# Kernel tuning notes

Measured on AMD Instinct MI355X. Metric: run time of the kernel, lower is better.

Reference implementation:

```python
import jax, jax.numpy as jnp
import numpy as np

SCALE = 0.125  # 1/sqrt(d_k), d_k = 64


def setup_inputs() -> dict:
    key = jax.random.key(0)
    kq, kk, kv, kp = jax.random.split(key, 4)
    H, B, L, T, D = 16, 4, 1024, 1024, 64
    return {
        "query": jax.random.normal(kq, (H, B, L, D), dtype=jnp.float32),
        "key": jax.random.normal(kk, (H, B, T, D), dtype=jnp.float32),
        "value": jax.random.normal(kv, (H, B, T, D), dtype=jnp.float32),
        "prev_attention": jax.random.normal(kp, (H, B, L, T), dtype=jnp.float32),
    }


def reference(query, key, value, prev_attention):
    # scores: [h, b, l, t]
    scores = jnp.einsum("hblk,hbtk->hblt", query, key) * SCALE
    scores = scores + prev_attention
    attention = jax.nn.softmax(scores, axis=-1)
    # dropout disabled (rate 0.0) for deterministic reference
    output = jnp.einsum("hblt,hbtv->hblv", attention, value)
    return (output, attention)
```

## Files before the change

kernel.cpp:

```cpp
#include <hip/hip_runtime.h>

#define SCALE 0.125f

constexpr int L_ = 1024, T_ = 1024, D_ = 64, HB_ = 64;

using f32x4 = __attribute__((ext_vector_type(4))) float;
using half8 = __attribute__((ext_vector_type(8))) _Float16;
using half4 = __attribute__((ext_vector_type(4))) _Float16;

__global__ __launch_bounds__(256) void cvt_k(const float* __restrict__ k,
                                             _Float16* __restrict__ kh) {
  const size_t i = ((size_t)blockIdx.x * 256 + threadIdx.x) * 8;
  f32x4 a = *(const f32x4*)(k + i);
  f32x4 b = *(const f32x4*)(k + i + 4);
  half8 h;
#pragma unroll
  for (int e = 0; e < 4; ++e) {
    h[e] = (_Float16)a[e];
    h[4 + e] = (_Float16)b[e];
  }
  *(half8*)(kh + i) = h;
}

__global__ __launch_bounds__(256) void cvt_v(const float* __restrict__ v,
                                             _Float16* __restrict__ vh) {
  __shared__ _Float16 ts[64][136];
  const int tid = threadIdx.x;
  const int hb = blockIdx.y;
  const int t0 = blockIdx.x * 128;
  {
    const int tr = tid >> 1, dh = (tid & 1) * 32;
    const float* p = v + ((size_t)hb * T_ + t0 + tr) * D_ + dh;
#pragma unroll
    for (int i = 0; i < 8; ++i) {
      f32x4 r = *(const f32x4*)(p + i * 4);
#pragma unroll
      for (int e = 0; e < 4; ++e) ts[dh + i * 4 + e][tr] = (_Float16)r[e];
    }
  }
  __syncthreads();
  {
    const int d = tid >> 2, tq = (tid & 3) * 32;
    _Float16* qo = vh + ((size_t)hb * D_ + d) * T_ + t0 + tq;
#pragma unroll
    for (int i = 0; i < 4; ++i)
      *(half8*)(qo + i * 8) = *(const half8*)&ts[d][tq + i * 8];
  }
}

__global__ __launch_bounds__(512) void zpass(
    const float* __restrict__ q, const _Float16* __restrict__ Kh,
    const float* __restrict__ prev, float* __restrict__ out,
    float* __restrict__ att) {
  __shared__ __align__(16) _Float16 Ks[1024][70];
  __shared__ __align__(16) _Float16 El[8][16][72];

  const int ltile = blockIdx.x;
  const int hb    = blockIdx.y;
  const int tid = threadIdx.x;
  const int w = tid >> 6, l = tid & 63, l15 = l & 15, lg = l >> 4;
  const int qrow = ltile * 128 + w * 16 + l15;

  const _Float16* kbase = Kh + (size_t)hb * T_ * D_;

  {
    const int srow = tid >> 2, scol = (tid & 3) * 16;
#pragma unroll
    for (int rep = 0; rep < 8; ++rep) {
      const int r = rep * 128 + srow;
      half8 a = *(const half8*)(kbase + (size_t)r * D_ + scol);
      half8 b = *(const half8*)(kbase + (size_t)r * D_ + scol + 8);
      *(half8*)&Ks[r][scol] = a;
      *(half8*)&Ks[r][scol + 8] = b;
    }
  }

  half8 qb2[2];
  {
    const float* qp = q + ((size_t)hb * L_ + qrow) * D_ + lg * 8;
#pragma unroll
    for (int f = 0; f < 2; ++f)
#pragma unroll
      for (int e = 0; e < 8; ++e) qb2[f][e] = (_Float16)qp[f * 32 + e];
  }

  const float* prow = prev + ((size_t)hb * L_ + qrow) * (size_t)T_;
  const int cr = l >> 2, j = l & 3;
  _Float16* eprow =
      (_Float16*)(att +
                  ((size_t)hb * L_ + ltile * 128 + w * 16 + cr) * (size_t)T_) +
      T_;

  f32x4 pb[2][4];
  auto pload = [&](int c, int s) {
#pragma unroll
    for (int nt = 0; nt < 4; ++nt)
      pb[s][nt] = *(const f32x4*)(prow + c * 64 + nt * 16 + lg * 4);
  };
  pload(0, 0);
  pload(1, 1);

  __syncthreads();

  float zsum = 0.f;

#pragma unroll 2
  for (int c = 0; c < 16; ++c) {
    f32x4 pvv[4];
#pragma unroll
    for (int nt = 0; nt < 4; ++nt) pvv[nt] = pb[c & 1][nt];
    if (c < 14) pload(c + 2, c & 1);

#pragma unroll
    for (int nt = 0; nt < 4; ++nt) {
      const int trow = c * 64 + nt * 16 + l15;
      half8 ka0 = *(const half8*)&Ks[trow][lg * 8];
      half8 ka1 = *(const half8*)&Ks[trow][32 + lg * 8];
      f32x4 acc = {0.f, 0.f, 0.f, 0.f};
      acc = __builtin_amdgcn_mfma_f32_16x16x32_f16(ka0, qb2[0], acc, 0, 0, 0);
      acc = __builtin_amdgcn_mfma_f32_16x16x32_f16(ka1, qb2[1], acc, 0, 0, 0);

      float e0 = __expf(acc[0] * SCALE + pvv[nt][0]);
      float e1 = __expf(acc[1] * SCALE + pvv[nt][1]);
      float e2 = __expf(acc[2] * SCALE + pvv[nt][2]);
      float e3 = __expf(acc[3] * SCALE + pvv[nt][3]);
      zsum += (e0 + e1) + (e2 + e3);
      half4 ev;
      ev[0] = (_Float16)e0; ev[1] = (_Float16)e1;
      ev[2] = (_Float16)e2; ev[3] = (_Float16)e3;
      *(half4*)&El[w][l15][nt * 16 + lg * 4] = ev;
    }

    half8 ha = *(const half8*)&El[w][cr][j * 8];
    half8 hb2 = *(const half8*)&El[w][cr][32 + j * 8];
    *(half8*)(eprow + c * 64 + j * 8) = ha;
    *(half8*)(eprow + c * 64 + 32 + j * 8) = hb2;
  }

  zsum += __shfl_xor(zsum, 16, 64);
  zsum += __shfl_xor(zsum, 32, 64);
  if (lg == 0) out[((size_t)hb * L_ + qrow) * (size_t)D_] = 1.0f / zsum;
}

__global__ __launch_bounds__(512) void pvpass(
    const _Float16* __restrict__ Vh, float* __restrict__ out,
    float* __restrict__ att) {
  __shared__ __align__(16) _Float16 Vt[64][1030];

  const int ltile = blockIdx.x;
  const int hb    = blockIdx.y;
  const int tid = threadIdx.x;
  const int w = tid >> 6, l = tid & 63, l15 = l & 15, lg = l >> 4;
  const int qrow = ltile * 128 + w * 16 + l15;

  const _Float16* vbh = Vh + (size_t)hb * D_ * T_;

  {
    const int d = tid >> 3, tq = (tid & 7) * 8;
#pragma unroll
    for (int rep = 0; rep < 16; ++rep) {
      const int t = rep * 64 + tq;
      *(half8*)&Vt[d][t] = *(const half8*)(vbh + (size_t)d * T_ + t);
    }
  }

  float* arow = att + ((size_t)hb * L_ + qrow) * (size_t)T_;
  const _Float16* erow = (const _Float16*)arow + T_;
  const float rzq = out[((size_t)hb * L_ + qrow) * (size_t)D_];

  half8 eb[4][2];
  auto eload = [&](int c, int s) {
    eb[s][0] = *(const half8*)(erow + c * 64 + lg * 8);
    eb[s][1] = *(const half8*)(erow + c * 64 + 32 + lg * 8);
  };
  eload(0, 0); eload(1, 1); eload(2, 2); eload(3, 3);

  __syncthreads();

  f32x4 oacc[4];
#pragma unroll
  for (int nd = 0; nd < 4; ++nd) oacc[nd] = (f32x4){0.f, 0.f, 0.f, 0.f};

#pragma unroll 4
  for (int c = 0; c < 16; ++c) {
    half8 e0 = eb[c & 3][0], e1 = eb[c & 3][1];
    if (c < 12) eload(c + 4, c & 3);

#pragma unroll
    for (int ks = 0; ks < 2; ++ks) {
      half8 ef = ks ? e1 : e0;
      f32x4 s0, s1;
      half8 af;
#pragma unroll
      for (int e = 0; e < 4; ++e) {
        float v0 = (float)ef[e] * rzq;
        float v1 = (float)ef[4 + e] * rzq;
        s0[e] = v0; s1[e] = v1;
        af[e] = (_Float16)v0;
        af[4 + e] = (_Float16)v1;
      }
      *(f32x4*)(arow + c * 64 + ks * 32 + lg * 8) = s0;
      *(f32x4*)(arow + c * 64 + ks * 32 + lg * 8 + 4) = s1;

#pragma unroll
      for (int nd = 0; nd < 4; ++nd) {
        half8 vb =
            *(const half8*)&Vt[nd * 16 + l15][c * 64 + ks * 32 + lg * 8];
        oacc[nd] =
            __builtin_amdgcn_mfma_f32_16x16x32_f16(af, vb, oacc[nd], 0, 0, 0);
      }
    }
  }

  float* outw =
      out + ((size_t)hb * L_ + ltile * 128 + w * 16 + lg * 4) * (size_t)D_;
#pragma unroll
  for (int nd = 0; nd < 4; ++nd)
#pragma unroll
    for (int i = 0; i < 4; ++i)
      outw[(size_t)i * D_ + nd * 16 + l15] = oacc[nd][i];
}

extern "C" void kernel_launch(void* const* d_in, const int* in_sizes, int n_in,
                              void* d_out, int out_size, void* d_ws,
                              size_t ws_size, hipStream_t stream) {
  const float* q    = (const float*)d_in[0];
  const float* k    = (const float*)d_in[1];
  const float* v    = (const float*)d_in[2];
  const float* prev = (const float*)d_in[3];

  float* out = (float*)d_out;
  float* att = out + (size_t)HB_ * L_ * D_;

  const size_t KV_ELEMS = (size_t)HB_ * T_ * D_;
  _Float16* Kh = (_Float16*)d_ws;
  _Float16* Vh = Kh + KV_ELEMS;

  cvt_k<<<(int)(KV_ELEMS / (256 * 8)), 256, 0, stream>>>(k, Kh);
  cvt_v<<<dim3(T_ / 128, HB_), 256, 0, stream>>>(v, Vh);

  zpass<<<dim3(L_ / 128, HB_), 512, 0, stream>>>(q, Kh, prev, out, att);
  pvpass<<<dim3(L_ / 128, HB_), 512, 0, stream>>>(Vh, out, att);
}
```

Before: 259.1 us.

## Fuse softmax-normalize and PV into one two-pass kernel, fold K conversion in

New measurement: 228.0 us. 1.14x faster.

```diff
diff --git a/kernel.cpp b/kernel.cpp
--- a/kernel.cpp
+++ b/kernel.cpp
@@ -7,20 +7,6 @@
 using f32x4 = __attribute__((ext_vector_type(4))) float;
 using half8 = __attribute__((ext_vector_type(8))) _Float16;
 using half4 = __attribute__((ext_vector_type(4))) _Float16;
-
-__global__ __launch_bounds__(256) void cvt_k(const float* __restrict__ k,
-                                             _Float16* __restrict__ kh) {
-  const size_t i = ((size_t)blockIdx.x * 256 + threadIdx.x) * 8;
-  f32x4 a = *(const f32x4*)(k + i);
-  f32x4 b = *(const f32x4*)(k + i + 4);
-  half8 h;
-#pragma unroll
-  for (int e = 0; e < 4; ++e) {
-    h[e] = (_Float16)a[e];
-    h[4 + e] = (_Float16)b[e];
-  }
-  *(half8*)(kh + i) = h;
-}
 
 __global__ __launch_bounds__(256) void cvt_v(const float* __restrict__ v,
                                              _Float16* __restrict__ vh) {
@@ -48,10 +34,10 @@
   }
 }
 
-__global__ __launch_bounds__(512) void zpass(
-    const float* __restrict__ q, const _Float16* __restrict__ Kh,
-    const float* __restrict__ prev, float* __restrict__ out,
-    float* __restrict__ att) {
+__global__ __launch_bounds__(512) void attn_all(
+    const float* __restrict__ q, const float* __restrict__ kk,
+    const _Float16* __restrict__ Vh, const float* __restrict__ prev,
+    float* __restrict__ out, float* __restrict__ att) {
   __shared__ __align__(16) _Float16 Ks[1024][70];
   __shared__ __align__(16) _Float16 El[8][16][72];
 
@@ -61,17 +47,25 @@
   const int w = tid >> 6, l = tid & 63, l15 = l & 15, lg = l >> 4;
   const int qrow = ltile * 128 + w * 16 + l15;
 
-  const _Float16* kbase = Kh + (size_t)hb * T_ * D_;
-
   {
     const int srow = tid >> 2, scol = (tid & 3) * 16;
+    const float* kp0 = kk + (size_t)hb * T_ * D_;
 #pragma unroll
     for (int rep = 0; rep < 8; ++rep) {
       const int r = rep * 128 + srow;
-      half8 a = *(const half8*)(kbase + (size_t)r * D_ + scol);
-      half8 b = *(const half8*)(kbase + (size_t)r * D_ + scol + 8);
-      *(half8*)&Ks[r][scol] = a;
-      *(half8*)&Ks[r][scol + 8] = b;
+      const float* p = kp0 + (size_t)r * D_ + scol;
+      f32x4 a = *(const f32x4*)(p);
+      f32x4 b = *(const f32x4*)(p + 4);
+      f32x4 cc = *(const f32x4*)(p + 8);
+      f32x4 d = *(const f32x4*)(p + 12);
+      half8 h0, h1;
+#pragma unroll
+      for (int e = 0; e < 4; ++e) {
+        h0[e] = (_Float16)a[e];  h0[4 + e] = (_Float16)b[e];
+        h1[e] = (_Float16)cc[e]; h1[4 + e] = (_Float16)d[e];
+      }
+      *(half8*)&Ks[r][scol] = h0;
+      *(half8*)&Ks[r][scol + 8] = h1;
     }
   }
 
@@ -85,11 +79,6 @@
   }
 
   const float* prow = prev + ((size_t)hb * L_ + qrow) * (size_t)T_;
-  const int cr = l >> 2, j = l & 3;
-  _Float16* eprow =
-      (_Float16*)(att +
-                  ((size_t)hb * L_ + ltile * 128 + w * 16 + cr) * (size_t)T_) +
-      T_;
 
   f32x4 pb[2][4];
   auto pload = [&](int c, int s) {
@@ -97,11 +86,11 @@
     for (int nt = 0; nt < 4; ++nt)
       pb[s][nt] = *(const f32x4*)(prow + c * 64 + nt * 16 + lg * 4);
   };
+
+  __syncthreads();
+
   pload(0, 0);
   pload(1, 1);
-
-  __syncthreads();
-
   float zsum = 0.f;
 
 #pragma unroll 2
@@ -119,96 +108,71 @@
       f32x4 acc = {0.f, 0.f, 0.f, 0.f};
       acc = __builtin_amdgcn_mfma_f32_16x16x32_f16(ka0, qb2[0], acc, 0, 0, 0);
       acc = __builtin_amdgcn_mfma_f32_16x16x32_f16(ka1, qb2[1], acc, 0, 0, 0);
-
-      float e0 = __expf(acc[0] * SCALE + pvv[nt][0]);
-      float e1 = __expf(acc[1] * SCALE + pvv[nt][1]);
-      float e2 = __expf(acc[2] * SCALE + pvv[nt][2]);
-      float e3 = __expf(acc[3] * SCALE + pvv[nt][3]);
-      zsum += (e0 + e1) + (e2 + e3);
-      half4 ev;
-      ev[0] = (_Float16)e0; ev[1] = (_Float16)e1;
-      ev[2] = (_Float16)e2; ev[3] = (_Float16)e3;
-      *(half4*)&El[w][l15][nt * 16 + lg * 4] = ev;
-    }
-
-    half8 ha = *(const half8*)&El[w][cr][j * 8];
-    half8 hb2 = *(const half8*)&El[w][cr][32 + j * 8];
-    *(half8*)(eprow + c * 64 + j * 8) = ha;
-    *(half8*)(eprow + c * 64 + 32 + j * 8) = hb2;
+      zsum += __expf(acc[0] * SCALE + pvv[nt][0]);
+      zsum += __expf(acc[1] * SCALE + pvv[nt][1]);
+      zsum += __expf(acc[2] * SCALE + pvv[nt][2]);
+      zsum += __expf(acc[3] * SCALE + pvv[nt][3]);
+    }
   }
 
   zsum += __shfl_xor(zsum, 16, 64);
   zsum += __shfl_xor(zsum, 32, 64);
-  if (lg == 0) out[((size_t)hb * L_ + qrow) * (size_t)D_] = 1.0f / zsum;
-}
-
-__global__ __launch_bounds__(512) void pvpass(
-    const _Float16* __restrict__ Vh, float* __restrict__ out,
-    float* __restrict__ att) {
-  __shared__ __align__(16) _Float16 Vt[64][1030];
-
-  const int ltile = blockIdx.x;
-  const int hb    = blockIdx.y;
-  const int tid = threadIdx.x;
-  const int w = tid >> 6, l = tid & 63, l15 = l & 15, lg = l >> 4;
-  const int qrow = ltile * 128 + w * 16 + l15;
+  const float rzq = 1.0f / zsum;
 
   const _Float16* vbh = Vh + (size_t)hb * D_ * T_;
-
-  {
-    const int d = tid >> 3, tq = (tid & 7) * 8;
-#pragma unroll
-    for (int rep = 0; rep < 16; ++rep) {
-      const int t = rep * 64 + tq;
-      *(half8*)&Vt[d][t] = *(const half8*)(vbh + (size_t)d * T_ + t);
-    }
-  }
-
   float* arow = att + ((size_t)hb * L_ + qrow) * (size_t)T_;
-  const _Float16* erow = (const _Float16*)arow + T_;
-  const float rzq = out[((size_t)hb * L_ + qrow) * (size_t)D_];
-
-  half8 eb[4][2];
-  auto eload = [&](int c, int s) {
-    eb[s][0] = *(const half8*)(erow + c * 64 + lg * 8);
-    eb[s][1] = *(const half8*)(erow + c * 64 + 32 + lg * 8);
-  };
-  eload(0, 0); eload(1, 1); eload(2, 2); eload(3, 3);
-
-  __syncthreads();
+
+  pload(0, 0);
+  pload(1, 1);
 
   f32x4 oacc[4];
 #pragma unroll
   for (int nd = 0; nd < 4; ++nd) oacc[nd] = (f32x4){0.f, 0.f, 0.f, 0.f};
 
-#pragma unroll 4
+#pragma unroll 2
   for (int c = 0; c < 16; ++c) {
-    half8 e0 = eb[c & 3][0], e1 = eb[c & 3][1];
-    if (c < 12) eload(c + 4, c & 3);
+    half8 vr[8];
+#pragma unroll
+    for (int ks = 0; ks < 2; ++ks)
+#pragma unroll
+      for (int nd = 0; nd < 4; ++nd)
+        vr[ks * 4 + nd] = *(const half8*)(vbh + (size_t)(nd * 16 + l15) * T_ +
+                                          c * 64 + ks * 32 + lg * 8);
+
+    f32x4 pvv[4];
+#pragma unroll
+    for (int nt = 0; nt < 4; ++nt) pvv[nt] = pb[c & 1][nt];
+    if (c < 14) pload(c + 2, c & 1);
+
+#pragma unroll
+    for (int nt = 0; nt < 4; ++nt) {
+      const int trow = c * 64 + nt * 16 + l15;
+      half8 ka0 = *(const half8*)&Ks[trow][lg * 8];
+      half8 ka1 = *(const half8*)&Ks[trow][32 + lg * 8];
+      f32x4 acc = {0.f, 0.f, 0.f, 0.f};
+      acc = __builtin_amdgcn_mfma_f32_16x16x32_f16(ka0, qb2[0], acc, 0, 0, 0);
+      acc = __builtin_amdgcn_mfma_f32_16x16x32_f16(ka1, qb2[1], acc, 0, 0, 0);
+
+      f32x4 s;
+      s[0] = __expf(acc[0] * SCALE + pvv[nt][0]) * rzq;
+      s[1] = __expf(acc[1] * SCALE + pvv[nt][1]) * rzq;
+      s[2] = __expf(acc[2] * SCALE + pvv[nt][2]) * rzq;
+      s[3] = __expf(acc[3] * SCALE + pvv[nt][3]) * rzq;
+      *(f32x4*)(arow + c * 64 + nt * 16 + lg * 4) = s;
+
+      half4 ev;
+      ev[0] = (_Float16)s[0]; ev[1] = (_Float16)s[1];
+      ev[2] = (_Float16)s[2]; ev[3] = (_Float16)s[3];
+      *(half4*)&El[w][l15][nt * 16 + lg * 4] = ev;
+    }
 
 #pragma unroll
     for (int ks = 0; ks < 2; ++ks) {
-      half8 ef = ks ? e1 : e0;
-      f32x4 s0, s1;
-      half8 af;
-#pragma unroll
-      for (int e = 0; e < 4; ++e) {
-        float v0 = (float)ef[e] * rzq;
-        float v1 = (float)ef[4 + e] * rzq;
-        s0[e] = v0; s1[e] = v1;
-        af[e] = (_Float16)v0;
-        af[4 + e] = (_Float16)v1;
-      }
-      *(f32x4*)(arow + c * 64 + ks * 32 + lg * 8) = s0;
-      *(f32x4*)(arow + c * 64 + ks * 32 + lg * 8 + 4) = s1;
-
-#pragma unroll
-      for (int nd = 0; nd < 4; ++nd) {
-        half8 vb =
-            *(const half8*)&Vt[nd * 16 + l15][c * 64 + ks * 32 + lg * 8];
-        oacc[nd] =
-            __builtin_amdgcn_mfma_f32_16x16x32_f16(af, vb, oacc[nd], 0, 0, 0);
-      }
+      half8 af = *(const half8*)&El[w][l15][ks * 32 + lg * 8];
+#pragma unroll
+      for (int nd = 0; nd < 4; ++nd)
+        oacc[nd] = __builtin_amdgcn_mfma_f32_16x16x32_f16(af, vr[ks * 4 + nd],
+                                                          oacc[nd], 0, 0, 0);
     }
   }
 
@@ -232,13 +196,8 @@
   float* out = (float*)d_out;
   float* att = out + (size_t)HB_ * L_ * D_;
 
-  const size_t KV_ELEMS = (size_t)HB_ * T_ * D_;
-  _Float16* Kh = (_Float16*)d_ws;
-  _Float16* Vh = Kh + KV_ELEMS;
-
-  cvt_k<<<(int)(KV_ELEMS / (256 * 8)), 256, 0, stream>>>(k, Kh);
+  _Float16* Vh = (_Float16*)d_ws;
+
   cvt_v<<<dim3(T_ / 128, HB_), 256, 0, stream>>>(v, Vh);
-
-  zpass<<<dim3(L_ / 128, HB_), 512, 0, stream>>>(q, Kh, prev, out, att);
-  pvpass<<<dim3(L_ / 128, HB_), 512, 0, stream>>>(Vh, out, att);
+  attn_all<<<dim3(L_ / 128, HB_), 512, 0, stream>>>(q, k, Vh, prev, out, att);
 }
```
